# Kernel tuning notes

Measured on AMD Instinct MI355X. Metric: run time of the kernel, lower is better.

## Reference

```python
import jax, jax.numpy as jnp
import numpy as np

B, T, F, H, L, OUT = 256, 168, 8, 512, 2, 24


def setup_inputs() -> dict:
    key = jax.random.key(0)
    ks = jax.random.split(key, 32)
    s = 1.0 / np.sqrt(H)  # torch LSTM/Linear init scale
    d = {"src": jax.random.normal(ks[0], (B, T, F), jnp.float32)}
    i = 1
    for pre in ("e", "d"):
        for l, in_dim in enumerate((F, H)):
            d[f"{pre}W_ih{l}"] = jax.random.normal(ks[i], (4 * H, in_dim), jnp.float32) * s; i += 1
            d[f"{pre}W_hh{l}"] = jax.random.normal(ks[i], (4 * H, H), jnp.float32) * s; i += 1
            d[f"{pre}b_ih{l}"] = jax.random.normal(ks[i], (4 * H,), jnp.float32) * s; i += 1
            d[f"{pre}b_hh{l}"] = jax.random.normal(ks[i], (4 * H,), jnp.float32) * s; i += 1
    d["fc_W"] = jax.random.normal(ks[i], (F, H), jnp.float32) * s
    d["fc_b"] = jax.random.normal(ks[i + 1], (F,), jnp.float32) * s
    return d


def _cell(x, h, c, Wih, Whh, bih, bhh):
    # single torch-style LSTM cell step; gate order i, f, g, o
    g = x @ Wih.T + bih + h @ Whh.T + bhh  # [B, 4H]
    i, f, gg, o = jnp.split(g, 4, axis=-1)
    c = jax.nn.sigmoid(f) * c + jax.nn.sigmoid(i) * jnp.tanh(gg)
    h = jax.nn.sigmoid(o) * jnp.tanh(c)
    return h, c


def _lstm_scan(x, Wih, Whh, bih, bhh):
    # x: [B, T, D] -> outputs [B, T, H], final (h, c)
    b = x.shape[0]
    h0 = jnp.zeros((b, H), x.dtype)
    c0 = jnp.zeros((b, H), x.dtype)
    xg = jnp.einsum('btd,gd->btg', x, Wih) + bih  # precompute input projections

    def step(carry, xg_t):
        h, c = carry
        g = xg_t + h @ Whh.T + bhh
        i, f, gg, o = jnp.split(g, 4, axis=-1)
        c = jax.nn.sigmoid(f) * c + jax.nn.sigmoid(i) * jnp.tanh(gg)
        h = jax.nn.sigmoid(o) * jnp.tanh(c)
        return (h, c), h

    (hT, cT), ys = jax.lax.scan(step, (h0, c0), jnp.swapaxes(xg, 0, 1))
    return jnp.swapaxes(ys, 0, 1), hT, cT


def reference(src, eW_ih0, eW_hh0, eb_ih0, eb_hh0, eW_ih1, eW_hh1, eb_ih1, eb_hh1,
              dW_ih0, dW_hh0, db_ih0, db_hh0, dW_ih1, dW_hh1, db_ih1, db_hh1,
              fc_W, fc_b):
    enc = [(eW_ih0, eW_hh0, eb_ih0, eb_hh0), (eW_ih1, eW_hh1, eb_ih1, eb_hh1)]
    dec = [(dW_ih0, dW_hh0, db_ih0, db_hh0), (dW_ih1, dW_hh1, db_ih1, db_hh1)]

    # encoder: stacked LSTM over input window, keep per-layer final (h, c)
    y = src
    hs, cs = [], []
    for (Wih, Whh, bih, bhh) in enc:
        y, h, c = _lstm_scan(y, Wih, Whh, bih, bhh)
        hs.append(h)
        cs.append(c)

    def step(carry, _):
        hs, cs, x = carry
        inp = x
        nh, nc = [], []
        for l, (Wih, Whh, bih, bhh) in enumerate(dec):
            h, c = _cell(inp, hs[l], cs[l], Wih, Whh, bih, bhh)
            nh.append(h)
            nc.append(c)
            inp = h
        pred = inp @ fc_W.T + fc_b  # [B, F]
        return (tuple(nh), tuple(nc), pred), pred

    carry0 = (tuple(hs), tuple(cs), src[:, -1, :])
    _, preds = jax.lax.scan(step, carry0, None, length=OUT)  # [OUT, B, F]
    return jnp.swapaxes(preds, 0, 1)  # [B, OUT, F]
```

## Files before the change

kernel.cpp:

```cpp
#include <hip/hip_runtime.h>
#include <hip/hip_bf16.h>

typedef __hip_bfloat16 bf16;
typedef __attribute__((ext_vector_type(8))) short short8;
typedef __attribute__((ext_vector_type(4))) short short4v;
typedef __attribute__((ext_vector_type(4))) float f32x4;

#define NBLK 192
#define SMEM_BYTES 147456
#define W0_STRIDE 1152

__device__ __forceinline__ float sigm(float x) { return 1.0f / (1.0f + __expf(-x)); }

__device__ __forceinline__ short f2bf(float f) {
    union { float f; unsigned int u; } v; v.f = f;
    unsigned int r = v.u + 0x7fffu + ((v.u >> 16) & 1u);
    return (short)(r >> 16);
}

__device__ __forceinline__ void store_short_wt(bf16* p, short v) {
    asm volatile("global_store_short %0, %1, off sc0 sc1"
                 :: "v"(p), "v"((int)(unsigned short)v) : "memory");
}
__device__ __forceinline__ void store_dword_wt(float* p, float v) {
    asm volatile("global_store_dword %0, %1, off sc0 sc1"
                 :: "v"(p), "v"(v) : "memory");
}
__device__ __forceinline__ void store_dword_wt_u(unsigned* p, unsigned v) {
    asm volatile("global_store_dword %0, %1, off sc0 sc1"
                 :: "v"(p), "v"(v) : "memory");
}
__device__ __forceinline__ unsigned poll_dword_wt(const unsigned* p) {
    unsigned v;
    asm volatile("global_load_dword %0, %1, off sc0 sc1\n\ts_waitcnt vmcnt(0)"
                 : "=v"(v) : "v"(p) : "memory");
    return v;
}
__device__ __forceinline__ short8 load_b16x8_wt(const bf16* p) {
    short8 v;
    asm volatile("global_load_dwordx4 %0, %1, off sc0 sc1"
                 : "=v"(v) : "v"(p) : "memory");
    return v;
}
__device__ __forceinline__ float load_f32_wt(const float* p) {
    float v;
    asm volatile("global_load_dword %0, %1, off sc0 sc1"
                 : "=v"(v) : "v"(p) : "memory");
    return v;
}
__device__ __forceinline__ void vmcnt0() {
    asm volatile("s_waitcnt vmcnt(0)" ::: "memory");
}
__device__ __forceinline__ void ldrain() {
    vmcnt0();
    __builtin_amdgcn_sched_barrier(0);
}

#define WS_H0      0x000000
#define WS_H1      0x0C0000
#define WS_PART    0x180000
#define WS_CNT     0x1C0000
#define WS_XBF     0x1D0000
#define WS_W       0x280000
#define WS_EWIH0   0xE80000
#define WS_DWIH0   0xE88000
#define WS_ZERO_BYTES 0x1D0000

struct CvtEntry { const float* s; bf16* d; int n; };
struct CvtArgs  { CvtEntry e[9]; };

__global__ __launch_bounds__(256) void convert_kernel(CvtArgs a)
{
    CvtEntry en = a.e[blockIdx.y];
    int n4 = en.n >> 2;
    const float4* s4 = (const float4*)en.s;
    short4v* d4 = (short4v*)en.d;
    for (int i = blockIdx.x * blockDim.x + threadIdx.x; i < n4;
         i += gridDim.x * blockDim.x) {
        float4 f = s4[i];
        short4v o;
        o[0] = f2bf(f.x); o[1] = f2bf(f.y); o[2] = f2bf(f.z); o[3] = f2bf(f.w);
        d4[i] = o;
    }
}

__global__ void init_kernel(unsigned int* ws)
{
    const int total = WS_ZERO_BYTES / 4;
    for (int i = blockIdx.x * blockDim.x + threadIdx.x; i < total;
         i += gridDim.x * blockDim.x)
        ws[i] = 0u;
}

struct KArgs {
    const bf16 *xbf;
    const bf16 *eWhh0, *eWih1, *eWhh1, *dWhh0, *dWih1, *dWhh1, *eWih0, *dWih0;
    const float *ebih0, *ebhh0, *ebih1, *ebhh1, *dbih0, *dbhh0, *dbih1, *dbhh1;
    const float *fcW, *fcb;
    bf16 *h0base, *h1base;
    float *partials;
    unsigned *cnt;
    float *outp;
};

__device__ __forceinline__ void pollw(const unsigned* baseA, unsigned tgtA,
                                      const unsigned* baseB, unsigned tgtB, int nB,
                                      int tid)
{
    if (tid < 64) {
        const unsigned* pA = (tid < 32) ? baseA + tid * 32 : nullptr;
        const unsigned* pB = (tid < nB) ? baseB + tid * 32 : nullptr;
        for (;;) {
            int ok = 1;
            if (pA) ok &= (poll_dword_wt(pA) >= tgtA) ? 1 : 0;
            if (pB) ok &= (poll_dword_wt(pB) >= tgtB) ? 1 : 0;
            if (__all(ok)) break;
            __builtin_amdgcn_s_sleep(1);
        }
    }
    __syncthreads();
}

__device__ __forceinline__ void publish(unsigned* mycnt, unsigned val, int tid)
{
    vmcnt0();
    __syncthreads();
    if (tid == 0) store_dword_wt_u(mycnt, val);
}

__device__ __forceinline__ void load_w0(char* lw, const bf16* Whh, const bf16* Wih, int j0, int tid)
{
    for (int u = tid; u < 64 * 68; u += 512) {
        int row = u / 68, uc = u - row * 68;
        int n = ((row >> 4) << 9) + j0 + (row & 15);
        int colel = uc << 3;
        short8 v = {0, 0, 0, 0, 0, 0, 0, 0};
        if (colel < 512)       v = *(const short8*)(Whh + (size_t)n * 512 + colel);
        else if (colel == 512) v = *(const short8*)(Wih + (size_t)n * 8);
        int off = row * W0_STRIDE + uc * 16;
        if (uc < 64) off ^= (row & 7) << 4;
        *(short8*)(lw + off) = v;
    }
}
__device__ __forceinline__ void load_w1(char* lw, const bf16* Wih, const bf16* Whh, int j0, int tid)
{
    for (int u = tid; u < 64 * 128; u += 512) {
        int row = u >> 7, uc = u & 127;
        int n = ((row >> 4) << 9) + j0 + (row & 15);
        int colel = uc << 3;
        short8 v;
        if (colel < 512) v = *(const short8*)(Wih + (size_t)n * 512 + colel);
        else             v = *(const short8*)(Whh + (size_t)n * 512 + (colel - 512));
        *(short8*)(lw + ((row * 2048 + uc * 16) ^ ((row & 7) << 4))) = v;
    }
}

template<bool DEC>
__device__ __forceinline__ void l0_step(
    const bf16* __restrict__ h0cur, bf16* __restrict__ h0nxt,
    const bf16* __restrict__ xbf, int s,
    const float* __restrict__ partials, const float* __restrict__ fcb,
    float* __restrict__ outp, int t,
    char* lw, bf16* lxs,
    float* cst, const float* bsum,
    int m0, int j0, int jb, int tid)
{
    const int w = tid >> 6;
    const int l = tid & 63, lr = l & 15, lg = l >> 4;

    if (DEC) {
        #pragma unroll
        for (int p = 0; p < 2; ++p) {
            int e = p * 512 + tid, mlo = e >> 3, f = e & 7;
            if (t == 0) {
                lxs[mlo * 8 + f] = xbf[((size_t)(m0 + mlo) * 168 + 167) * 8 + f];
            } else {
                float pv[32];
                #pragma unroll
                for (int q = 0; q < 32; ++q)
                    pv[q] = load_f32_wt(partials + q * 2048 + (m0 + mlo) * 8 + f);
                ldrain();
                float sacc = fcb[f];
                #pragma unroll
                for (int q = 0; q < 32; ++q) sacc += pv[q];
                if (jb == 0) outp[(size_t)(m0 + mlo) * 192 + (t - 1) * 8 + f] = sacc;
                ((short*)lxs)[mlo * 8 + f] = f2bf(sacc);
            }
        }
        __syncthreads();
    }

    const bf16* arow = h0cur + ((size_t)(m0 + w * 16 + lr) << 9) + lg * 8;
    short8 afr[16];
    #pragma unroll
    for (int kcg = 0; kcg < 16; ++kcg)
        afr[kcg] = load_b16x8_wt(arow + kcg * 32);
    short8 ax = {0, 0, 0, 0, 0, 0, 0, 0};
    if (lg == 0) {
        if (DEC) ax = *(const short8*)(lxs + (w * 16 + lr) * 8);
        else     ax = *(const short8*)(xbf + ((size_t)(m0 + w * 16 + lr) * 168 + s) * 8);
    }
    ldrain();

    f32x4 acc[4];
    #pragma unroll
    for (int g = 0; g < 4; ++g) acc[g] = (f32x4){0.f, 0.f, 0.f, 0.f};

    #pragma unroll
    for (int kcg = 0; kcg < 17; ++kcg) {
        #pragma unroll
        for (int g = 0; g < 4; ++g) {
            int wrow = g * 16 + lr;
            int off = wrow * W0_STRIDE + kcg * 64 + lg * 16;
            if (kcg < 16) off ^= (wrow & 7) << 4;
            short8 bfr = *(const short8*)(lw + off);
            short8 av = (kcg < 16) ? afr[kcg] : ax;
            acc[g] = __builtin_amdgcn_mfma_f32_16x16x32_bf16(av, bfr, acc[g], 0, 0, 0);
        }
    }

    #pragma unroll
    for (int r = 0; r < 4; ++r) {
        float gi = acc[0][r] + bsum[0];
        float gf = acc[1][r] + bsum[1];
        float gg = acc[2][r] + bsum[2];
        float go = acc[3][r] + bsum[3];
        float cv = sigm(gf) * cst[r] + sigm(gi) * tanhf(gg);
        float hv = sigm(go) * tanhf(cv);
        cst[r] = cv;
        store_short_wt(h0nxt + ((size_t)(m0 + w * 16 + lg * 4 + r) << 9) + j0 + lr, f2bf(hv));
    }
}

template<bool DEC>
__device__ __forceinline__ void l1_step(
    const bf16* __restrict__ h0src, const bf16* __restrict__ h1prev, bf16* __restrict__ h1nxt,
    float* __restrict__ partials, const float* __restrict__ wf,
    char* lw, float* lgl,
    float* cst, const float* bsum,
    int m0, int j0, int jb, int tid)
{
    const int w = tid >> 6, mt = w & 3, kh = w >> 2;
    const int l = tid & 63, lr = l & 15, lg = l >> 4;
    const bf16* A = (kh == 0) ? h0src : h1prev;
    const int colbase = (kh == 0) ? 0 : 1024;

    const bf16* arow = A + ((size_t)(m0 + mt * 16 + lr) << 9) + lg * 8;
    short8 afr[16];
    #pragma unroll
    for (int kc = 0; kc < 16; ++kc)
        afr[kc] = load_b16x8_wt(arow + kc * 32);
    ldrain();

    f32x4 acc[4];
    #pragma unroll
    for (int g = 0; g < 4; ++g) acc[g] = (f32x4){0.f, 0.f, 0.f, 0.f};

    #pragma unroll
    for (int kc = 0; kc < 16; ++kc) {
        #pragma unroll
        for (int g = 0; g < 4; ++g) {
            int wrow = g * 16 + lr;
            short8 bfr = *(const short8*)(lw + ((wrow * 2048 + colbase + kc * 64 + lg * 16) ^ ((wrow & 7) << 4)));
            acc[g] = __builtin_amdgcn_mfma_f32_16x16x32_bf16(afr[kc], bfr, acc[g], 0, 0, 0);
        }
    }

    if (kh == 1) {
        #pragma unroll
        for (int g = 0; g < 4; ++g)
            #pragma unroll
            for (int r = 0; r < 4; ++r)
                lgl[(g * 64 + mt * 16 + lg * 4 + r) * 16 + lr] = acc[g][r];
    }
    __syncthreads();
    if (kh == 0) {
        #pragma unroll
        for (int r = 0; r < 4; ++r) {
            int mrow = mt * 16 + lg * 4 + r;
            float gi = acc[0][r] + lgl[(0 * 64 + mrow) * 16 + lr] + bsum[0];
            float gf = acc[1][r] + lgl[(1 * 64 + mrow) * 16 + lr] + bsum[1];
            float gg = acc[2][r] + lgl[(2 * 64 + mrow) * 16 + lr] + bsum[2];
            float go = acc[3][r] + lgl[(3 * 64 + mrow) * 16 + lr] + bsum[3];
            float cv = sigm(gf) * cst[r] + sigm(gi) * tanhf(gg);
            float hv = sigm(go) * tanhf(cv);
            cst[r] = cv;
            store_short_wt(h1nxt + ((size_t)(m0 + mrow) << 9) + j0 + lr, f2bf(hv));
            if (DEC) {
                #pragma unroll
                for (int f = 0; f < 8; ++f) {
                    float v = hv * wf[f];
                    v += __shfl_xor(v, 1); v += __shfl_xor(v, 2);
                    v += __shfl_xor(v, 4); v += __shfl_xor(v, 8);
                    if (lr == f)
                        store_dword_wt(partials + jb * 2048 + (m0 + mrow) * 8 + f, v);
                }
            }
        }
    }
}

__global__ __launch_bounds__(512, 2) void net_kernel(KArgs a)
{
    extern __shared__ char smem[];
    const int tid = threadIdx.x;
    const int bid = blockIdx.x;
    const int role = (bid < 64) ? 0 : 1;
    const int sub = role == 0 ? bid : bid - 64;
    const int jb = sub & 31;
    const int grp = sub >> 5;
    const int m0 = (role == 0) ? grp * 128 : grp * 64;
    const int j0 = jb * 16;
    const int mh = (role == 0) ? grp : (grp >> 1);

    unsigned* cnt = a.cnt;
    unsigned* mycnt = cnt + ((role == 0) ? (grp * 32 + jb) : (64 + grp * 32 + jb)) * 32;
    const unsigned* l0grp = cnt + (mh * 32) * 32;
    const unsigned* l1cat = cnt + (64 + 2 * mh * 32) * 32;
    const unsigned* l1grp = cnt + (64 + grp * 32) * 32;

    char* lw  = smem;
    float* lgl = (float*)(smem + 131072);
    bf16* lxs  = (bf16*)(smem + 64 * W0_STRIDE);

    bf16* B0[3] = { a.h0base, a.h0base + 131072, a.h0base + 262144 };
    bf16* B1[3] = { a.h1base, a.h1base + 131072, a.h1base + 262144 };

    if (role == 0) load_w0(lw, a.eWhh0, a.eWih0, j0, tid);
    else           load_w1(lw, a.eWih1, a.eWhh1, j0, tid);

    float bsum[4];
    {
        const float* bi = role == 0 ? a.ebih0 : a.ebih1;
        const float* bh = role == 0 ? a.ebhh0 : a.ebhh1;
        #pragma unroll
        for (int g2 = 0; g2 < 4; ++g2) {
            int n = (g2 << 9) + j0 + (tid & 15);
            bsum[g2] = bi[n] + bh[n];
        }
    }
    float cst[4] = {0.f, 0.f, 0.f, 0.f};
    float wf[8] = {0.f, 0.f, 0.f, 0.f, 0.f, 0.f, 0.f, 0.f};
    __syncthreads();

    if (role == 0) {
        for (int p = 0; p < 192; ++p) {
            const bool dec = p >= 168;
            if (p == 168) {
                load_w0(lw, a.dWhh0, a.dWih0, j0, tid);
                #pragma unroll
                for (int g2 = 0; g2 < 4; ++g2) {
                    int n = (g2 << 9) + j0 + (tid & 15);
                    bsum[g2] = a.dbih0[n] + a.dbhh0[n];
                }
                __syncthreads();
            }
            unsigned t1 = (unsigned)p;
            unsigned t2 = (p >= 169) ? (unsigned)p : (p >= 2 ? (unsigned)(p - 2) : 0u);
            pollw(l0grp, t1, l1cat, t2, 64, tid);

            if (!dec)
                l0_step<false>(B0[(p + 2) % 3], B0[p % 3], a.xbf, p,
                               nullptr, nullptr, nullptr, 0,
                               lw, lxs, cst, bsum, m0, j0, jb, tid);
            else
                l0_step<true>(B0[(p + 2) % 3], B0[p % 3], a.xbf, 0,
                              a.partials, a.fcb, a.outp, p - 168,
                              lw, lxs, cst, bsum, m0, j0, jb, tid);
            publish(mycnt, (unsigned)(p + 1), tid);
        }
        if (jb == 0) {
            pollw(l1cat, 192u, l1cat, 192u, 64, tid);
            #pragma unroll
            for (int p2 = 0; p2 < 2; ++p2) {
                int e = p2 * 512 + tid, mlo = e >> 3, f = e & 7;
                float pv[32];
                #pragma unroll
                for (int q = 0; q < 32; ++q)
                    pv[q] = load_f32_wt(a.partials + q * 2048 + (m0 + mlo) * 8 + f);
                ldrain();
                float sacc = a.fcb[f];
                #pragma unroll
                for (int q = 0; q < 32; ++q) sacc += pv[q];
                a.outp[(size_t)(m0 + mlo) * 192 + 23 * 8 + f] = sacc;
            }
        }
    } else {
        for (int q = 0; q < 192; ++q) {
            const bool dec = q >= 168;
            if (q == 168) {
                load_w1(lw, a.dWih1, a.dWhh1, j0, tid);
                #pragma unroll
                for (int g2 = 0; g2 < 4; ++g2) {
                    int n = (g2 << 9) + j0 + (tid & 15);
                    bsum[g2] = a.dbih1[n] + a.dbhh1[n];
                }
                #pragma unroll
                for (int f = 0; f < 8; ++f) wf[f] = a.fcW[f * 512 + j0 + (tid & 15)];
                __syncthreads();
            }
            pollw(l0grp, (unsigned)(q + 1), l1grp, (unsigned)q, 32, tid);

            if (!dec)
                l1_step<false>(B0[q % 3], B1[(q + 2) % 3], B1[q % 3],
                               nullptr, nullptr, lw, lgl, cst, bsum, m0, j0, jb, tid);
            else
                l1_step<true>(B0[q % 3], B1[(q + 2) % 3], B1[q % 3],
                              a.partials, wf, lw, lgl, cst, bsum, m0, j0, jb, tid);
            publish(mycnt, (unsigned)(q + 1), tid);
        }
    }
}

extern "C" void kernel_launch(void* const* d_in, const int* in_sizes, int n_in,
                              void* d_out, int out_size, void* d_ws, size_t ws_size,
                              hipStream_t stream)
{
    (void)in_sizes; (void)n_in; (void)out_size; (void)ws_size;
    const float* src   = (const float*)d_in[0];
    const float* eWih0 = (const float*)d_in[1];
    const float* eWhh0 = (const float*)d_in[2];
    const float* ebih0 = (const float*)d_in[3];
    const float* ebhh0 = (const float*)d_in[4];
    const float* eWih1 = (const float*)d_in[5];
    const float* eWhh1 = (const float*)d_in[6];
    const float* ebih1 = (const float*)d_in[7];
    const float* ebhh1 = (const float*)d_in[8];
    const float* dWih0 = (const float*)d_in[9];
    const float* dWhh0 = (const float*)d_in[10];
    const float* dbih0 = (const float*)d_in[11];
    const float* dbhh0 = (const float*)d_in[12];
    const float* dWih1 = (const float*)d_in[13];
    const float* dWhh1 = (const float*)d_in[14];
    const float* dbih1 = (const float*)d_in[15];
    const float* dbhh1 = (const float*)d_in[16];
    const float* fcW   = (const float*)d_in[17];
    const float* fcb   = (const float*)d_in[18];

    char* ws = (char*)d_ws;
    const int NH = 2048 * 512;

    CvtArgs ca;
    ca.e[0] = { eWhh0, (bf16*)(ws + WS_W + 0x000000), NH };
    ca.e[1] = { eWih1, (bf16*)(ws + WS_W + 0x200000), NH };
    ca.e[2] = { eWhh1, (bf16*)(ws + WS_W + 0x400000), NH };
    ca.e[3] = { dWhh0, (bf16*)(ws + WS_W + 0x600000), NH };
    ca.e[4] = { dWih1, (bf16*)(ws + WS_W + 0x800000), NH };
    ca.e[5] = { dWhh1, (bf16*)(ws + WS_W + 0xA00000), NH };
    ca.e[6] = { eWih0, (bf16*)(ws + WS_EWIH0), 2048 * 8 };
    ca.e[7] = { dWih0, (bf16*)(ws + WS_DWIH0), 2048 * 8 };
    ca.e[8] = { src,   (bf16*)(ws + WS_XBF),   256 * 168 * 8 };

    KArgs ka;
    ka.xbf   = (const bf16*)(ws + WS_XBF);
    ka.eWhh0 = (const bf16*)(ws + WS_W + 0x000000);
    ka.eWih1 = (const bf16*)(ws + WS_W + 0x200000);
    ka.eWhh1 = (const bf16*)(ws + WS_W + 0x400000);
    ka.dWhh0 = (const bf16*)(ws + WS_W + 0x600000);
    ka.dWih1 = (const bf16*)(ws + WS_W + 0x800000);
    ka.dWhh1 = (const bf16*)(ws + WS_W + 0xA00000);
    ka.eWih0 = (const bf16*)(ws + WS_EWIH0);
    ka.dWih0 = (const bf16*)(ws + WS_DWIH0);
    ka.ebih0 = ebih0; ka.ebhh0 = ebhh0; ka.ebih1 = ebih1; ka.ebhh1 = ebhh1;
    ka.dbih0 = dbih0; ka.dbhh0 = dbhh0; ka.dbih1 = dbih1; ka.dbhh1 = dbhh1;
    ka.fcW = fcW; ka.fcb = fcb;
    ka.h0base = (bf16*)(ws + WS_H0);
    ka.h1base = (bf16*)(ws + WS_H1);
    ka.partials = (float*)(ws + WS_PART);
    ka.cnt      = (unsigned*)(ws + WS_CNT);
    ka.outp     = (float*)d_out;

    hipFuncSetAttribute((const void*)net_kernel,
                        hipFuncAttributeMaxDynamicSharedMemorySize, SMEM_BYTES);

    convert_kernel<<<dim3(128, 9), dim3(256), 0, stream>>>(ca);
    init_kernel<<<dim3(512), dim3(256), 0, stream>>>((unsigned int*)ws);
    net_kernel<<<dim3(NBLK), dim3(512), SMEM_BYTES, stream>>>(ka);
}
```

Before: 2.303 ms.

## Halve block to 256 threads with two M-tiles per wave and split A-load waits

Reduces the persistent LSTM kernel from 512 to 256 threads per block, so each wave now computes two 16-row M tiles and reuses every LDS weight fragment across both. A-fragment global loads are split with a partial vmcnt wait, so the first half of the MFMAs can start while the rest are still arriving. The poller now tracks per-lane completion and takes a configurable lane count. In exchange there are fewer waves to hide latency and more registers per thread (two accumulator sets, 32 A fragments), which could cause spills or lower throughput per CU.

After: 2.303 ms. About the same (-0.0%).

```diff
diff --git a/kernel.cpp b/kernel.cpp
--- a/kernel.cpp
+++ b/kernel.cpp
@@ -103,18 +103,18 @@
     float *outp;
 };
 
-__device__ __forceinline__ void pollw(const unsigned* baseA, unsigned tgtA,
+__device__ __forceinline__ void pollw(const unsigned* baseA, unsigned tgtA, int nA,
                                       const unsigned* baseB, unsigned tgtB, int nB,
                                       int tid)
 {
     if (tid < 64) {
-        const unsigned* pA = (tid < 32) ? baseA + tid * 32 : nullptr;
+        const unsigned* pA = (tid < nA) ? baseA + tid * 32 : nullptr;
         const unsigned* pB = (tid < nB) ? baseB + tid * 32 : nullptr;
+        bool dA = (pA == nullptr), dB = (pB == nullptr);
         for (;;) {
-            int ok = 1;
-            if (pA) ok &= (poll_dword_wt(pA) >= tgtA) ? 1 : 0;
-            if (pB) ok &= (poll_dword_wt(pB) >= tgtB) ? 1 : 0;
-            if (__all(ok)) break;
+            if (!dA && poll_dword_wt(pA) >= tgtA) dA = true;
+            if (!dB && poll_dword_wt(pB) >= tgtB) dB = true;
+            if (__all(dA && dB)) break;
             __builtin_amdgcn_s_sleep(1);
         }
     }
@@ -130,7 +130,7 @@
 
 __device__ __forceinline__ void load_w0(char* lw, const bf16* Whh, const bf16* Wih, int j0, int tid)
 {
-    for (int u = tid; u < 64 * 68; u += 512) {
+    for (int u = tid; u < 64 * 68; u += 256) {
         int row = u / 68, uc = u - row * 68;
         int n = ((row >> 4) << 9) + j0 + (row & 15);
         int colel = uc << 3;
@@ -144,7 +144,7 @@
 }
 __device__ __forceinline__ void load_w1(char* lw, const bf16* Wih, const bf16* Whh, int j0, int tid)
 {
-    for (int u = tid; u < 64 * 128; u += 512) {
+    for (int u = tid; u < 64 * 128; u += 256) {
         int row = u >> 7, uc = u & 127;
         int n = ((row >> 4) << 9) + j0 + (row & 15);
         int colel = uc << 3;
@@ -167,11 +167,12 @@
 {
     const int w = tid >> 6;
     const int l = tid & 63, lr = l & 15, lg = l >> 4;
+    const short8 z8 = {0, 0, 0, 0, 0, 0, 0, 0};
 
     if (DEC) {
         #pragma unroll
-        for (int p = 0; p < 2; ++p) {
-            int e = p * 512 + tid, mlo = e >> 3, f = e & 7;
+        for (int p = 0; p < 4; ++p) {
+            int e = p * 256 + tid, mlo = e >> 3, f = e & 7;
             if (t == 0) {
                 lxs[mlo * 8 + f] = xbf[((size_t)(m0 + mlo) * 168 + 167) * 8 + f];
             } else {
@@ -190,45 +191,80 @@
         __syncthreads();
     }
 
-    const bf16* arow = h0cur + ((size_t)(m0 + w * 16 + lr) << 9) + lg * 8;
-    short8 afr[16];
-    #pragma unroll
-    for (int kcg = 0; kcg < 16; ++kcg)
-        afr[kcg] = load_b16x8_wt(arow + kcg * 32);
-    short8 ax = {0, 0, 0, 0, 0, 0, 0, 0};
-    if (lg == 0) {
-        if (DEC) ax = *(const short8*)(lxs + (w * 16 + lr) * 8);
-        else     ax = *(const short8*)(xbf + ((size_t)(m0 + w * 16 + lr) * 168 + s) * 8);
-    }
-    ldrain();
-
-    f32x4 acc[4];
-    #pragma unroll
-    for (int g = 0; g < 4; ++g) acc[g] = (f32x4){0.f, 0.f, 0.f, 0.f};
-
-    #pragma unroll
-    for (int kcg = 0; kcg < 17; ++kcg) {
+    const bf16* ar0 = h0cur + ((size_t)(m0 + (w * 2 + 0) * 16 + lr) << 9) + lg * 8;
+    const bf16* ar1 = h0cur + ((size_t)(m0 + (w * 2 + 1) * 16 + lr) << 9) + lg * 8;
+    short8 a0[16], a1[16];
+    #pragma unroll
+    for (int kcg = 0; kcg < 16; ++kcg) {
+        a0[kcg] = load_b16x8_wt(ar0 + kcg * 32);
+        a1[kcg] = load_b16x8_wt(ar1 + kcg * 32);
+    }
+    short8 ax0 = z8, ax1 = z8;
+    if (!DEC) {
+        ax0 = load_b16x8_wt(xbf + ((size_t)(m0 + (w * 2 + 0) * 16 + lr) * 168 + s) * 8);
+        ax1 = load_b16x8_wt(xbf + ((size_t)(m0 + (w * 2 + 1) * 16 + lr) * 168 + s) * 8);
+    }
+
+    asm volatile("s_waitcnt vmcnt(%0)" :: "i"(DEC ? 16 : 18) : "memory");
+    __builtin_amdgcn_sched_barrier(0);
+
+    f32x4 acc0[4], acc1[4];
+    #pragma unroll
+    for (int g = 0; g < 4; ++g) { acc0[g] = (f32x4){0,0,0,0}; acc1[g] = (f32x4){0,0,0,0}; }
+
+    #pragma unroll
+    for (int kcg = 0; kcg < 8; ++kcg) {
         #pragma unroll
         for (int g = 0; g < 4; ++g) {
             int wrow = g * 16 + lr;
-            int off = wrow * W0_STRIDE + kcg * 64 + lg * 16;
-            if (kcg < 16) off ^= (wrow & 7) << 4;
-            short8 bfr = *(const short8*)(lw + off);
-            short8 av = (kcg < 16) ? afr[kcg] : ax;
-            acc[g] = __builtin_amdgcn_mfma_f32_16x16x32_bf16(av, bfr, acc[g], 0, 0, 0);
-        }
-    }
-
-    #pragma unroll
-    for (int r = 0; r < 4; ++r) {
-        float gi = acc[0][r] + bsum[0];
-        float gf = acc[1][r] + bsum[1];
-        float gg = acc[2][r] + bsum[2];
-        float go = acc[3][r] + bsum[3];
-        float cv = sigm(gf) * cst[r] + sigm(gi) * tanhf(gg);
-        float hv = sigm(go) * tanhf(cv);
-        cst[r] = cv;
-        store_short_wt(h0nxt + ((size_t)(m0 + w * 16 + lg * 4 + r) << 9) + j0 + lr, f2bf(hv));
+            short8 bfr = *(const short8*)(lw + ((wrow * W0_STRIDE + kcg * 64 + lg * 16) ^ ((wrow & 7) << 4)));
+            acc0[g] = __builtin_amdgcn_mfma_f32_16x16x32_bf16(a0[kcg], bfr, acc0[g], 0, 0, 0);
+            acc1[g] = __builtin_amdgcn_mfma_f32_16x16x32_bf16(a1[kcg], bfr, acc1[g], 0, 0, 0);
+        }
+    }
+    ldrain();
+
+    if (!DEC) {
+        if (lg != 0) { ax0 = z8; ax1 = z8; }
+    } else {
+        if (lg == 0) {
+            ax0 = *(const short8*)(lxs + ((w * 2 + 0) * 16 + lr) * 8);
+            ax1 = *(const short8*)(lxs + ((w * 2 + 1) * 16 + lr) * 8);
+        }
+    }
+
+    #pragma unroll
+    for (int kcg = 8; kcg < 16; ++kcg) {
+        #pragma unroll
+        for (int g = 0; g < 4; ++g) {
+            int wrow = g * 16 + lr;
+            short8 bfr = *(const short8*)(lw + ((wrow * W0_STRIDE + kcg * 64 + lg * 16) ^ ((wrow & 7) << 4)));
+            acc0[g] = __builtin_amdgcn_mfma_f32_16x16x32_bf16(a0[kcg], bfr, acc0[g], 0, 0, 0);
+            acc1[g] = __builtin_amdgcn_mfma_f32_16x16x32_bf16(a1[kcg], bfr, acc1[g], 0, 0, 0);
+        }
+    }
+    #pragma unroll
+    for (int g = 0; g < 4; ++g) {
+        int wrow = g * 16 + lr;
+        short8 bfr = *(const short8*)(lw + wrow * W0_STRIDE + 1024 + lg * 16);
+        acc0[g] = __builtin_amdgcn_mfma_f32_16x16x32_bf16(ax0, bfr, acc0[g], 0, 0, 0);
+        acc1[g] = __builtin_amdgcn_mfma_f32_16x16x32_bf16(ax1, bfr, acc1[g], 0, 0, 0);
+    }
+
+    #pragma unroll
+    for (int mi = 0; mi < 2; ++mi) {
+        #pragma unroll
+        for (int r = 0; r < 4; ++r) {
+            float gi = (mi ? acc1[0][r] : acc0[0][r]) + bsum[0];
+            float gf = (mi ? acc1[1][r] : acc0[1][r]) + bsum[1];
+            float gg = (mi ? acc1[2][r] : acc0[2][r]) + bsum[2];
+            float go = (mi ? acc1[3][r] : acc0[3][r]) + bsum[3];
+            float cv = sigm(gf) * cst[mi * 4 + r] + sigm(gi) * tanhf(gg);
+            float hv = sigm(go) * tanhf(cv);
+            cst[mi * 4 + r] = cv;
+            store_short_wt(h0nxt + ((size_t)(m0 + (w * 2 + mi) * 16 + lg * 4 + r) << 9) + j0 + lr,
+                           f2bf(hv));
+        }
     }
 }
 
@@ -240,67 +276,89 @@
     float* cst, const float* bsum,
     int m0, int j0, int jb, int tid)
 {
-    const int w = tid >> 6, mt = w & 3, kh = w >> 2;
+    const int w = tid >> 6, kh = w >> 1, mp = w & 1;
     const int l = tid & 63, lr = l & 15, lg = l >> 4;
     const bf16* A = (kh == 0) ? h0src : h1prev;
     const int colbase = (kh == 0) ? 0 : 1024;
 
-    const bf16* arow = A + ((size_t)(m0 + mt * 16 + lr) << 9) + lg * 8;
-    short8 afr[16];
-    #pragma unroll
-    for (int kc = 0; kc < 16; ++kc)
-        afr[kc] = load_b16x8_wt(arow + kc * 32);
-    ldrain();
-
-    f32x4 acc[4];
-    #pragma unroll
-    for (int g = 0; g < 4; ++g) acc[g] = (f32x4){0.f, 0.f, 0.f, 0.f};
-
+    const bf16* ar0 = A + ((size_t)(m0 + (mp * 2 + 0) * 16 + lr) << 9) + lg * 8;
+    const bf16* ar1 = A + ((size_t)(m0 + (mp * 2 + 1) * 16 + lr) << 9) + lg * 8;
+    short8 a0[16], a1[16];
     #pragma unroll
     for (int kc = 0; kc < 16; ++kc) {
+        a0[kc] = load_b16x8_wt(ar0 + kc * 32);
+        a1[kc] = load_b16x8_wt(ar1 + kc * 32);
+    }
+    asm volatile("s_waitcnt vmcnt(16)" ::: "memory");
+    __builtin_amdgcn_sched_barrier(0);
+
+    f32x4 acc0[4], acc1[4];
+    #pragma unroll
+    for (int g = 0; g < 4; ++g) { acc0[g] = (f32x4){0,0,0,0}; acc1[g] = (f32x4){0,0,0,0}; }
+
+    #pragma unroll
+    for (int kc = 0; kc < 8; ++kc) {
         #pragma unroll
         for (int g = 0; g < 4; ++g) {
             int wrow = g * 16 + lr;
             short8 bfr = *(const short8*)(lw + ((wrow * 2048 + colbase + kc * 64 + lg * 16) ^ ((wrow & 7) << 4)));
-            acc[g] = __builtin_amdgcn_mfma_f32_16x16x32_bf16(afr[kc], bfr, acc[g], 0, 0, 0);
+            acc0[g] = __builtin_amdgcn_mfma_f32_16x16x32_bf16(a0[kc], bfr, acc0[g], 0, 0, 0);
+            acc1[g] = __builtin_amdgcn_mfma_f32_16x16x32_bf16(a1[kc], bfr, acc1[g], 0, 0, 0);
+        }
+    }
+    ldrain();
+    #pragma unroll
+    for (int kc = 8; kc < 16; ++kc) {
+        #pragma unroll
+        for (int g = 0; g < 4; ++g) {
+            int wrow = g * 16 + lr;
+            short8 bfr = *(const short8*)(lw + ((wrow * 2048 + colbase + kc * 64 + lg * 16) ^ ((wrow & 7) << 4)));
+            acc0[g] = __builtin_amdgcn_mfma_f32_16x16x32_bf16(a0[kc], bfr, acc0[g], 0, 0, 0);
+            acc1[g] = __builtin_amdgcn_mfma_f32_16x16x32_bf16(a1[kc], bfr, acc1[g], 0, 0, 0);
         }
     }
 
     if (kh == 1) {
         #pragma unroll
-        for (int g = 0; g < 4; ++g)
+        for (int mi = 0; mi < 2; ++mi)
             #pragma unroll
-            for (int r = 0; r < 4; ++r)
-                lgl[(g * 64 + mt * 16 + lg * 4 + r) * 16 + lr] = acc[g][r];
+            for (int g = 0; g < 4; ++g)
+                #pragma unroll
+                for (int r = 0; r < 4; ++r)
+                    lgl[(g * 64 + (mp * 2 + mi) * 16 + lg * 4 + r) * 16 + lr] =
+                        (mi ? acc1[g][r] : acc0[g][r]);
     }
     __syncthreads();
     if (kh == 0) {
         #pragma unroll
-        for (int r = 0; r < 4; ++r) {
-            int mrow = mt * 16 + lg * 4 + r;
-            float gi = acc[0][r] + lgl[(0 * 64 + mrow) * 16 + lr] + bsum[0];
-            float gf = acc[1][r] + lgl[(1 * 64 + mrow) * 16 + lr] + bsum[1];
-            float gg = acc[2][r] + lgl[(2 * 64 + mrow) * 16 + lr] + bsum[2];
-            float go = acc[3][r] + lgl[(3 * 64 + mrow) * 16 + lr] + bsum[3];
-            float cv = sigm(gf) * cst[r] + sigm(gi) * tanhf(gg);
-            float hv = sigm(go) * tanhf(cv);
-            cst[r] = cv;
-            store_short_wt(h1nxt + ((size_t)(m0 + mrow) << 9) + j0 + lr, f2bf(hv));
-            if (DEC) {
-                #pragma unroll
-                for (int f = 0; f < 8; ++f) {
-                    float v = hv * wf[f];
-                    v += __shfl_xor(v, 1); v += __shfl_xor(v, 2);
-                    v += __shfl_xor(v, 4); v += __shfl_xor(v, 8);
-                    if (lr == f)
-                        store_dword_wt(partials + jb * 2048 + (m0 + mrow) * 8 + f, v);
+        for (int mi = 0; mi < 2; ++mi) {
+            #pragma unroll
+            for (int r = 0; r < 4; ++r) {
+                int mrow = (mp * 2 + mi) * 16 + lg * 4 + r;
+                float gi = (mi ? acc1[0][r] : acc0[0][r]) + lgl[(0 * 64 + mrow) * 16 + lr] + bsum[0];
+                float gf = (mi ? acc1[1][r] : acc0[1][r]) + lgl[(1 * 64 + mrow) * 16 + lr] + bsum[1];
+                float gg = (mi ? acc1[2][r] : acc0[2][r]) + lgl[(2 * 64 + mrow) * 16 + lr] + bsum[2];
+                float go = (mi ? acc1[3][r] : acc0[3][r]) + lgl[(3 * 64 + mrow) * 16 + lr] + bsum[3];
+                float cv = sigm(gf) * cst[mi * 4 + r] + sigm(gi) * tanhf(gg);
+                float hv = sigm(go) * tanhf(cv);
+                cst[mi * 4 + r] = cv;
+                store_short_wt(h1nxt + ((size_t)(m0 + mrow) << 9) + j0 + lr, f2bf(hv));
+                if (DEC) {
+                    #pragma unroll
+                    for (int f = 0; f < 8; ++f) {
+                        float v = hv * wf[f];
+                        v += __shfl_xor(v, 1); v += __shfl_xor(v, 2);
+                        v += __shfl_xor(v, 4); v += __shfl_xor(v, 8);
+                        if (lr == f)
+                            store_dword_wt(partials + jb * 2048 + (m0 + mrow) * 8 + f, v);
+                    }
                 }
             }
         }
     }
 }
 
-__global__ __launch_bounds__(512, 2) void net_kernel(KArgs a)
+__global__ __launch_bounds__(256, 1) void net_kernel(KArgs a)
 {
     extern __shared__ char smem[];
     const int tid = threadIdx.x;
@@ -339,8 +397,8 @@
             bsum[g2] = bi[n] + bh[n];
         }
     }
-    float cst[4] = {0.f, 0.f, 0.f, 0.f};
-    float wf[8] = {0.f, 0.f, 0.f, 0.f, 0.f, 0.f, 0.f, 0.f};
+    float cst[8] = {0.f, 0.f, 0.f, 0.f, 0.f, 0.f, 0.f, 0.f};
+    float wf[8]  = {0.f, 0.f, 0.f, 0.f, 0.f, 0.f, 0.f, 0.f};
     __syncthreads();
 
     if (role == 0) {
@@ -357,7 +415,7 @@
             }
             unsigned t1 = (unsigned)p;
             unsigned t2 = (p >= 169) ? (unsigned)p : (p >= 2 ? (unsigned)(p - 2) : 0u);
-            pollw(l0grp, t1, l1cat, t2, 64, tid);
+            pollw(l0grp, t1, 32, l1cat, t2, 64, tid);
 
             if (!dec)
                 l0_step<false>(B0[(p + 2) % 3], B0[p % 3], a.xbf, p,
@@ -370,10 +428,10 @@
             publish(mycnt, (unsigned)(p + 1), tid);
         }
         if (jb == 0) {
-            pollw(l1cat, 192u, l1cat, 192u, 64, tid);
+            pollw(l1cat, 192u, 64, nullptr, 0u, 0, tid);
             #pragma unroll
-            for (int p2 = 0; p2 < 2; ++p2) {
-                int e = p2 * 512 + tid, mlo = e >> 3, f = e & 7;
+            for (int p2 = 0; p2 < 4; ++p2) {
+                int e = p2 * 256 + tid, mlo = e >> 3, f = e & 7;
                 float pv[32];
                 #pragma unroll
                 for (int q = 0; q < 32; ++q)
@@ -399,7 +457,7 @@
                 for (int f = 0; f < 8; ++f) wf[f] = a.fcW[f * 512 + j0 + (tid & 15)];
                 __syncthreads();
             }
-            pollw(l0grp, (unsigned)(q + 1), l1grp, (unsigned)q, 32, tid);
+            pollw(l0grp, (unsigned)(q + 1), 32, l1grp, (unsigned)q, 32, tid);
 
             if (!dec)
                 l1_step<false>(B0[q % 3], B1[(q + 2) % 3], B1[q % 3],
@@ -475,5 +533,5 @@
 
     convert_kernel<<<dim3(128, 9), dim3(256), 0, stream>>>(ca);
     init_kernel<<<dim3(512), dim3(256), 0, stream>>>((unsigned int*)ws);
-    net_kernel<<<dim3(NBLK), dim3(512), SMEM_BYTES, stream>>>(ka);
-}
+    net_kernel<<<dim3(NBLK), dim3(256), SMEM_BYTES, stream>>>(ka);
+}
```
